# Performance work log

Hardware: AMD Instinct MI355X
Metric: run time of the kernel (lower is better)

The kernel has to match this reference:

```python
import jax, jax.numpy as jnp
import numpy as np

# ---- hyperparameters (from args defaults) ----
TEMPERATURE = 0.07
ALPHA = 0.5
OT_EPSILON = 0.1
OT_ITERS = 20
HOLO_WEIGHT = 1.0
RKD_DISTANCE_WEIGHT = 1.0
RKD_ANGLE_WEIGHT = 2.0
GLOBAL_RKD_WEIGHT = 10.0
MATRYOSHKA_DIMS = [128, 768]
MATRYOSHKA_WEIGHTS = [1.0, 2.0]

B, N, H_S, H_T, D_REP = 64, 256, 768, 1024, 768


def l2norm(x, axis=-1):
    # F.normalize(p=2): x / max(||x||, eps)
    n = jnp.sqrt(jnp.sum(x * x, axis=axis, keepdims=True))
    return x / jnp.maximum(n, 1e-12)


def pairwise_distance(x):
    # [n, d] -> [n, n] squared-euclidean-style distances
    sq = jnp.sum(x * x, axis=1, keepdims=True)
    return sq + sq.T - 2.0 * (x @ x.T)


def huber(diff):
    a = jnp.abs(diff)
    return jnp.where(a < 1.0, 0.5 * a * a, a - 0.5)


def rkd_distance_loss(s, t):
    n = s.shape[0]
    mask = jnp.triu(jnp.ones((n, n), dtype=bool), k=1)
    cnt = jnp.sum(mask.astype(s.dtype))
    ds, dt = pairwise_distance(s), pairwise_distance(t)
    mean_s = jax.lax.stop_gradient(jnp.sum(jnp.where(mask, ds, 0.0)) / cnt) + 1e-8
    mean_t = jax.lax.stop_gradient(jnp.sum(jnp.where(mask, dt, 0.0)) / cnt) + 1e-8
    loss = huber(ds / mean_s - dt / mean_t)
    return jnp.sum(jnp.where(mask, loss, 0.0)) / cnt


def angle_potentials(x):
    # diffs[i, j] = x[j] - x[i]
    diffs = x[None, :, :] - x[:, None, :]
    e = diffs / (jnp.linalg.norm(diffs, axis=-1, keepdims=True) + 1e-8)
    return jnp.einsum('ijd,kjd->ijk', e, e)


def rkd_angle_loss(s, t):
    psi_s, psi_t = angle_potentials(s), angle_potentials(t)
    n = psi_s.shape[0]
    idx = jnp.arange(n)
    i, j, k = idx[:, None, None], idx[None, :, None], idx[None, None, :]
    mask = (i != j) & (i != k) & (j != k)  # exclude degenerate triplets
    cnt = jnp.sum(mask.astype(s.dtype))
    loss = huber(psi_s - psi_t)
    return jnp.sum(jnp.where(mask, loss, 0.0)) / cnt


def saliency_measure(h, temp=1.0):
    # softmax over token axis of hidden-state norms -> [B, N, 1]
    norms = jnp.linalg.norm(h, axis=-1)
    return jax.nn.softmax(norms / temp, axis=-1)[..., None]


def structure_matrix(z):
    zn = l2norm(z, axis=-1)
    return 1.0 - jnp.einsum('bnd,bmd->bnm', zn, zn)


def sinkhorn_knopp_log_domain(C, mu, nu):
    # C: [B, Ns, Nt]; mu: [B, Ns, 1]; nu: [B, Nt, 1]
    log_K = -C / OT_EPSILON
    log_mu = jnp.log(mu + 1e-8)
    log_nu = jnp.log(nu + 1e-8)
    u = jnp.zeros_like(mu)
    v = jnp.zeros_like(nu)
    for _ in range(OT_ITERS):
        u = log_mu - jax.scipy.special.logsumexp(
            log_K + jnp.swapaxes(v, 1, 2), axis=2, keepdims=True)
        v = log_nu - jax.scipy.special.logsumexp(
            jnp.swapaxes(log_K, 1, 2) + jnp.swapaxes(u, 1, 2),
            axis=2, keepdims=True)
    return jnp.exp(u + log_K + jnp.swapaxes(v, 1, 2))


def fused_gromov_wasserstein(z_s, z_t, proj_w, proj_b):
    mu = saliency_measure(z_s)   # [B, N, 1]
    nu = saliency_measure(z_t)   # [B, N, 1]
    C_s = structure_matrix(z_s)  # [B, N, N]
    C_t = structure_matrix(z_t)
    z_s_norm = l2norm(z_s @ proj_w + proj_b, axis=-1)
    z_t_norm = l2norm(z_t, axis=-1)
    M = 1.0 - jnp.einsum('bnd,bmd->bnm', z_s_norm, z_t_norm)
    Gamma = sinkhorn_knopp_log_domain(M, mu, nu)
    feat_loss = jnp.mean(jnp.sum(M * Gamma, axis=(1, 2)))
    Gamma_norm = Gamma / (jnp.sum(Gamma, axis=2, keepdims=True) + 1e-8)
    C_t_mapped = jnp.einsum('bnm,bmk,blk->bnl', Gamma_norm, C_t, Gamma_norm)
    w = jnp.einsum('bni,bmi->bnm', mu, mu)  # mu @ mu^T
    struct_loss = jnp.mean(jnp.sum((C_s - C_t_mapped) ** 2 * w, axis=(1, 2)))
    return (1.0 - ALPHA) * feat_loss + ALPHA * struct_loss


def cross_entropy_inbatch(scores):
    # labels = arange(B)
    logZ = jax.scipy.special.logsumexp(scores, axis=1)
    return jnp.mean(logZ - jnp.diagonal(scores))


def setup_inputs() -> dict:
    key = jax.random.key(0)
    ks = jax.random.split(key, 10)
    return {
        's_q_reps': jax.random.normal(ks[0], (B, D_REP), jnp.float32),
        's_p_reps': jax.random.normal(ks[1], (B, D_REP), jnp.float32),
        't_q_reps': jax.random.normal(ks[2], (B, D_REP), jnp.float32),
        't_p_reps': jax.random.normal(ks[3], (B, D_REP), jnp.float32),
        's_q_states': jax.random.normal(ks[4], (B, N, H_S), jnp.float32),
        's_p_states': jax.random.normal(ks[5], (B, N, H_S), jnp.float32),
        't_q_states': jax.random.normal(ks[6], (B, N, H_T), jnp.float32),
        't_p_states': jax.random.normal(ks[7], (B, N, H_T), jnp.float32),
        'proj_w': jax.random.normal(ks[8], (H_S, H_T), jnp.float32) * (H_S ** -0.5),
        'proj_b': jnp.zeros((H_T,), jnp.float32),
    }


def reference(s_q_reps, s_p_reps, t_q_reps, t_p_reps,
              s_q_states, s_p_states, t_q_states, t_p_states,
              proj_w, proj_b):
    # teacher outputs are computed under torch.no_grad()
    t_q_reps = jax.lax.stop_gradient(t_q_reps)
    t_p_reps = jax.lax.stop_gradient(t_p_reps)
    t_q_states = jax.lax.stop_gradient(t_q_states)
    t_p_states = jax.lax.stop_gradient(t_p_states)

    contrastive_acc = 0.0
    holo_acc = 0.0
    rkd_acc = 0.0
    for dim, dim_weight in zip(MATRYOSHKA_DIMS, MATRYOSHKA_WEIGHTS):
        s_q_slice = l2norm(s_q_reps[:, :dim])
        s_p_slice = l2norm(s_p_reps[:, :dim])
        scores = (s_q_slice @ s_p_slice.T) / TEMPERATURE
        contrastive_acc += dim_weight * cross_entropy_inbatch(scores)
        if dim <= 128:
            s_batch = jnp.concatenate([s_q_slice, s_p_slice], axis=0)
            t_batch = jnp.concatenate(
                [l2norm(t_q_reps[:, :dim]), l2norm(t_p_reps[:, :dim])], axis=0)
            loss_dist = rkd_distance_loss(s_batch, t_batch)
            loss_angle = rkd_angle_loss(s_batch, t_batch)
            rkd_val = (RKD_DISTANCE_WEIGHT * loss_dist
                       + RKD_ANGLE_WEIGHT * loss_angle)
            rkd_acc += GLOBAL_RKD_WEIGHT * rkd_val * 2.0
        else:
            loss_q = fused_gromov_wasserstein(s_q_states, t_q_states, proj_w, proj_b)
            loss_p = fused_gromov_wasserstein(s_p_states, t_p_states, proj_w, proj_b)
            holo_acc += HOLO_WEIGHT * 0.5 * (loss_q + loss_p)
    return contrastive_acc + holo_acc + rkd_acc
```

## Files before the change

kernel.cpp:

```cpp
#include <hip/hip_runtime.h>
#include <math.h>

#define NB   64
#define NN   256
#define HSS  768
#define HTT  1024
#define ROWS (NB*NN)
#define C2LOG 14.426950408889634f

typedef unsigned short u16;
typedef __attribute__((ext_vector_type(8))) short bf16x8;
typedef __attribute__((ext_vector_type(4))) float f32x4;

#define LIDX(r,c) (((r)<<8) + (((((c)>>3) + (r)) & 31)<<3) + ((c)&7))
#define EIDX(r,c) (((r)<<7) + (((((c)>>3) + (r)) & 15)<<3) + ((c)&7))

__device__ __forceinline__ void gl16(const u16* g, u16* l){
  __builtin_amdgcn_global_load_lds(
      (const __attribute__((address_space(1))) unsigned int*)g,
      (__attribute__((address_space(3))) unsigned int*)l,
      16, 0, 0);
}

static const size_t OFF_ACC   = 0;
static const size_t OFF_SQ128 = 16;
static const size_t OFF_SP128 = OFF_SQ128 + 64*128;
static const size_t OFF_TQ128 = OFF_SP128 + 64*128;
static const size_t OFF_TP128 = OFF_TQ128 + 64*128;
static const size_t OFF_SQ768 = OFF_TP128 + 64*128;
static const size_t OFF_SP768 = OFF_SQ768 + 64*768;
static const size_t OFF_DS    = OFF_SP768 + 64*768;
static const size_t OFF_DT    = OFF_DS + 128*128;
static const size_t OFF_CS    = OFF_DT + 128*128;
static const size_t OFF_MBF   = OFF_CS  + (size_t)2*NB*NN*NN;
static const size_t OFF_ZS_BF = OFF_MBF + (size_t)NB*NN*NN;
static const size_t OFF_ZT_BF = OFF_ZS_BF + (size_t)ROWS*HSS/2;
static const size_t OFF_WT_BF = OFF_ZT_BF + (size_t)ROWS*HTT/2;
static const size_t OFF_ZSP_BF= OFF_WT_BF + (size_t)HTT*HSS/2;
static const size_t OFF_GN_BF = OFF_ZSP_BF+ (size_t)ROWS*HTT/2;
static const size_t OFF_CT_BF = OFF_GN_BF + (size_t)NB*NN*NN;
static const size_t OFF_T_BF  = OFF_ZS_BF;
static const size_t OFF_NS    = OFF_CT_BF + (size_t)NB*NN*NN;
static const size_t OFF_NT    = OFF_NS + ROWS;
static const size_t OFF_MU    = OFF_NT + ROWS;
static const size_t OFF_NU    = OFF_MU + 2*ROWS;
static const size_t OFF_NSPP  = OFF_NU + 2*ROWS;


__device__ __forceinline__ float wred_sum(float v){
  #pragma unroll
  for(int o=32;o>0;o>>=1) v += __shfl_xor(v,o,64);
  return v;
}
__device__ __forceinline__ float wred_max(float v){
  #pragma unroll
  for(int o=32;o>0;o>>=1) v = fmaxf(v, __shfl_xor(v,o,64));
  return v;
}
__device__ __forceinline__ u16 f2bf(float f){
  unsigned u = __float_as_uint(f);
  unsigned r = (u + 0x7fffu + ((u>>16)&1u)) >> 16;
  return (u16)r;
}
__device__ __forceinline__ float bf2f(u16 h){
  return __uint_as_float(((unsigned)h)<<16);
}

__global__ __launch_bounds__(256) void k_l2norm_all(
    const float* __restrict__ sq, const float* __restrict__ sp,
    const float* __restrict__ tq, const float* __restrict__ tp,
    float* __restrict__ ws){
  int bid = blockIdx.x;
  int r = bid & 63;
  const float* in; float* out; int kuse;
  if(bid < 64)       { in = sq; out = ws + OFF_SQ128; kuse = 128; }
  else if(bid < 128) { in = sp; out = ws + OFF_SP128; kuse = 128; }
  else if(bid < 192) { in = tq; out = ws + OFF_TQ128; kuse = 128; }
  else if(bid < 256) { in = tp; out = ws + OFF_TP128; kuse = 128; }
  else if(bid < 320) { in = sq; out = ws + OFF_SQ768; kuse = 768; }
  else               { in = sp; out = ws + OFF_SP768; kuse = 768; }
  const float* row = in + (size_t)r*768;
  float ss = 0.f;
  for(int d=threadIdx.x; d<kuse; d+=256){ float x=row[d]; ss += x*x; }
  ss = wred_sum(ss);
  __shared__ float sm[4];
  if((threadIdx.x&63)==0) sm[threadIdx.x>>6]=ss;
  __syncthreads();
  float tot = sm[0]+sm[1]+sm[2]+sm[3];
  float inv = 1.f / fmaxf(sqrtf(tot), 1e-12f);
  for(int d=threadIdx.x; d<kuse; d+=256) out[(size_t)r*kuse + d] = row[d]*inv;
}

__global__ __launch_bounds__(512) void k_contrastive2(const float* __restrict__ ws,
    float* __restrict__ acc){
  int bid = blockIdx.x;
  int i = bid & 63;
  int big = bid >> 6;
  const float* q = ws + (big ? OFF_SQ768 : OFF_SQ128);
  const float* p = ws + (big ? OFF_SP768 : OFF_SP128);
  int dim = big ? 768 : 128;
  float weight = big ? 2.f : 1.f;
  int j = threadIdx.x & 63;
  int part = threadIdx.x >> 6;
  const float* qi = q + (size_t)i*dim;
  const float* pj = p + (size_t)j*dim;
  int seg = dim >> 3;
  int d0 = part*seg;
  float dot = 0.f;
  for(int d=d0; d<d0+seg; d+=4){
    float4 a = *(const float4*)(qi+d);
    float4 b = *(const float4*)(pj+d);
    dot = fmaf(a.x,b.x,dot);
    dot = fmaf(a.y,b.y,dot);
    dot = fmaf(a.z,b.z,dot);
    dot = fmaf(a.w,b.w,dot);
  }
  __shared__ float sm[8][64];
  sm[part][j] = dot;
  __syncthreads();
  if(part==0){
    float s = 0.f;
    #pragma unroll
    for(int k=0;k<8;k++) s += sm[k][j];
    s = s / 0.07f;
    float mx = wred_max(s);
    float e = expf(s - mx);
    float Z = wred_sum(e);
    float logZ = mx + logf(Z);
    float diag = __shfl(s, i, 64);
    if(j==0) atomicAdd(acc+0, weight*(logZ - diag)*(1.f/64.f));
  }
}

__global__ __launch_bounds__(256) void k_pack_cvt(
    const float* __restrict__ zs, const float* __restrict__ zt,
    u16* __restrict__ zsb, u16* __restrict__ ztb,
    float* __restrict__ ns, float* __restrict__ nt,
    const float* __restrict__ sb128, const float* __restrict__ tb128,
    float* __restrict__ ds, float* __restrict__ dt, float* __restrict__ acc)
{
  __shared__ float sm[2][2];
  int bid = blockIdx.x;
  if(bid < 8192){
    const float* in; u16* out; float* nrm; int K; int cb;
    if(bid < 4096){ in=zs; out=zsb; nrm=ns; K=HSS; cb=bid; }
    else          { in=zt; out=ztb; nrm=nt; K=HTT; cb=bid-4096; }
    int w = threadIdx.x >> 6, l = threadIdx.x & 63;
    int r = cb*4 + w;
    const float* row = in + (size_t)r*K;
    u16* orow = out + (size_t)r*K;
    float ss = 0.f;
    int nv = K >> 8;
    for(int i=0;i<nv;i++){
      int d = l*4 + i*256;
      float4 x = *(const float4*)(row + d);
      ushort4 o; o.x=f2bf(x.x); o.y=f2bf(x.y); o.z=f2bf(x.z); o.w=f2bf(x.w);
      *(ushort4*)(orow + d) = o;
      ss += x.x*x.x + x.y*x.y + x.z*x.z + x.w*x.w;
    }
    ss = wred_sum(ss);
    if(l==0) nrm[r] = sqrtf(ss);
    return;
  }
  {
    int r = bid - 8192;
    int c = threadIdx.x;
    float ms = 0.f, mt = 0.f;
    if(c < 128){
      const float* sr = sb128 + r*128; const float* sc = sb128 + c*128;
      const float* tr = tb128 + r*128; const float* tc = tb128 + c*128;
      float dot_s=0,ssr=0,ssc=0,dot_t=0,tsr=0,tsc=0;
      for(int d=0; d<128; d++){
        float a=sr[d], bb=sc[d]; dot_s += a*bb; ssr += a*a; ssc += bb*bb;
        float at=tr[d], bt=tc[d]; dot_t += at*bt; tsr += at*at; tsc += bt*bt;
      }
      float dv = ssr + ssc - 2.f*dot_s;
      float tv = tsr + tsc - 2.f*dot_t;
      ds[r*128+c] = dv; dt[r*128+c] = tv;
      ms = (c>r)? dv : 0.f;
      mt = (c>r)? tv : 0.f;
      ms = wred_sum(ms); mt = wred_sum(mt);
      if((c&63)==0){ sm[0][c>>6]=ms; sm[1][c>>6]=mt; }
    }
    __syncthreads();
    if(threadIdx.x==0){
      atomicAdd(acc+1, sm[0][0]+sm[0][1]);
      atomicAdd(acc+2, sm[1][0]+sm[1][1]);
    }
  }
}

__global__ __launch_bounds__(256) void k_small0(
    const float* __restrict__ ds, const float* __restrict__ dt,
    const float* __restrict__ ns, const float* __restrict__ nt,
    float* __restrict__ omu, float* __restrict__ onu, float* __restrict__ acc)
{
  __shared__ float sm[4], sm2[4];
  int bid = blockIdx.x;
  if(bid < 128){
    int r = bid, c = threadIdx.x;
    float mean_s = acc[1]*(1.f/8128.f) + 1e-8f;
    float mean_t = acc[2]*(1.f/8128.f) + 1e-8f;
    float h = 0.f;
    if(c < 128){
      if(c > r){
        float diff = ds[r*128+c]/mean_s - dt[r*128+c]/mean_t;
        float a = fabsf(diff);
        h = (a<1.f)? 0.5f*a*a : a-0.5f;
      }
      h = wred_sum(h);
      if((c&63)==0) sm[c>>6]=h;
    }
    __syncthreads();
    if(threadIdx.x==0) atomicAdd(acc+3, sm[0]+sm[1]);
    return;
  }
  {
    int b0 = bid - 128, n = threadIdx.x;
    const float* nrm = (b0 < NB) ? ns : nt;
    float* out = (b0 < NB) ? omu : onu;
    int b = b0 & 63;
    float x = nrm[b*NN+n];
    float mx = wred_max(x);
    if((n&63)==0) sm[n>>6]=mx;
    __syncthreads();
    mx = fmaxf(fmaxf(sm[0],sm[1]),fmaxf(sm[2],sm[3]));
    float e = expf(x-mx);
    float s = wred_sum(e);
    if((n&63)==0) sm2[n>>6]=s;
    __syncthreads();
    s = sm2[0]+sm2[1]+sm2[2]+sm2[3];
    out[b*NN+n] = e/s;
  }
}

#define RKD_LDS 65536
__global__ __launch_bounds__(256, 1) void k_rkd_angle_mfma(
    const float* __restrict__ sb, const float* __restrict__ tb,
    float* __restrict__ accp)
{
  extern __shared__ u16 eSh[];
  u16* Es = eSh;
  u16* Et = eSh + 128*128;
  const int j    = blockIdx.x >> 1;
  const int half = blockIdx.x & 1;
  const int tid = threadIdx.x;
  {
    const int i = tid >> 1, h = tid & 1;
    #pragma unroll
    for(int which=0; which<2; which++){
      const float* xb = which ? tb : sb;
      u16* E = which ? Et : Es;
      const float* xj = xb + j*128 + h*64;
      const float* xi = xb + i*128 + h*64;
      float ss = 0.f;
      #pragma unroll
      for(int d4=0; d4<16; d4++){
        float4 a = *(const float4*)(xj + d4*4);
        float4 b = *(const float4*)(xi + d4*4);
        float d0=a.x-b.x, d1=a.y-b.y, d2=a.z-b.z, d3=a.w-b.w;
        ss += d0*d0+d1*d1+d2*d2+d3*d3;
      }
      ss += __shfl_xor(ss, 1, 64);
      float inv = (i==j) ? 0.f : 1.f/(sqrtf(ss)+1e-8f);
      #pragma unroll
      for(int d4=0; d4<16; d4++){
        float4 a = *(const float4*)(xj + d4*4);
        float4 b = *(const float4*)(xi + d4*4);
        int c = h*64 + d4*4;
        E[EIDX(i,c+0)] = f2bf((a.x-b.x)*inv);
        E[EIDX(i,c+1)] = f2bf((a.y-b.y)*inv);
        E[EIDX(i,c+2)] = f2bf((a.z-b.z)*inv);
        E[EIDX(i,c+3)] = f2bf((a.w-b.w)*inv);
      }
    }
  }
  __syncthreads();
  const int w = tid >> 6, lane = tid & 63;
  const int q = lane >> 4, loc = lane & 15;
  float hsum = 0.f;
  #pragma unroll
  for(int ni=0; ni<4; ni++){
    const int cb = half*64 + ni*16;
    #pragma unroll
    for(int mi=0; mi<2; mi++){
      const int rb = w*32 + mi*16;
      f32x4 as_ = {0.f,0.f,0.f,0.f}, at_ = {0.f,0.f,0.f,0.f};
      #pragma unroll
      for(int k0=0; k0<128; k0+=32){
        int ra = rb + loc, rbn = cb + loc;
        int ca = k0 + q*8;
        bf16x8 aS = *(const bf16x8*)(Es + EIDX(ra, ca));
        bf16x8 bS = *(const bf16x8*)(Es + EIDX(rbn, ca));
        bf16x8 aT = *(const bf16x8*)(Et + EIDX(ra, ca));
        bf16x8 bT = *(const bf16x8*)(Et + EIDX(rbn, ca));
        as_ = __builtin_amdgcn_mfma_f32_16x16x32_bf16(aS, bS, as_, 0,0,0);
        at_ = __builtin_amdgcn_mfma_f32_16x16x32_bf16(aT, bT, at_, 0,0,0);
      }
      #pragma unroll
      for(int jj=0; jj<4; jj++){
        int row = rb + q*4 + jj, col = cb + loc;
        if(row != col){
          float d = as_[jj] - at_[jj];
          float a = fabsf(d);
          hsum += (a < 1.f) ? 0.5f*a*a : a - 0.5f;
        }
      }
    }
  }
  hsum = wred_sum(hsum);
  __syncthreads();
  float* red = (float*)eSh;
  if(lane==0) red[w] = hsum;
  __syncthreads();
  if(tid==0) atomicAdd(accp+4, red[0]+red[1]+red[2]+red[3]);
}

__global__ void k_wt(const float* __restrict__ W, u16* __restrict__ Wt){
  __shared__ float t[32][33];
  int k0 = blockIdx.y*32, n0 = blockIdx.x*32;
  int tx = threadIdx.x, ty = threadIdx.y;
  for(int r=0;r<32;r+=8) t[ty+r][tx] = W[(size_t)(k0+ty+r)*HTT + n0+tx];
  __syncthreads();
  for(int r=0;r<32;r+=8) Wt[(size_t)(n0+ty+r)*HSS + k0+tx] = f2bf(t[tx][ty+r]);
}

__global__ __launch_bounds__(256) void k_saliency2(const float* __restrict__ ns,
    const float* __restrict__ nt, float* __restrict__ omu, float* __restrict__ onu){
  int b0 = blockIdx.x, n = threadIdx.x;
  const float* nrm = (b0 < NB) ? ns : nt;
  float* out = (b0 < NB) ? omu : onu;
  int b = b0 & 63;
  float x = nrm[b*NN+n];
  float mx = wred_max(x);
  __shared__ float sm[4], sm2[4];
  if((n&63)==0) sm[n>>6]=mx;
  __syncthreads();
  mx = fmaxf(fmaxf(sm[0],sm[1]),fmaxf(sm[2],sm[3]));
  float e = expf(x-mx);
  float s = wred_sum(e);
  if((n&63)==0) sm2[n>>6]=s;
  __syncthreads();
  s = sm2[0]+sm2[1]+sm2[2]+sm2[3];
  out[b*NN+n] = e/s;
}

__global__ __launch_bounds__(256) void k_proj(
    const u16* __restrict__ A, const u16* __restrict__ B,
    u16* __restrict__ outB, const float* __restrict__ bias,
    float* __restrict__ nspp)
{
  __shared__ u16 As[128*32];
  __shared__ u16 Bs[128*32];

  int gx = gridDim.x, gy = gridDim.y;
  int flat = blockIdx.x + gx*blockIdx.y;
  int nwg  = gx*gy;
  int cpx  = nwg >> 3;
  int lg   = (flat & 7)*cpx + (flat >> 3);
  int bx   = lg % gx;
  int by   = lg / gx;

  int tid = threadIdx.x;
  int lane = tid & 63, w = tid >> 6;
  int m0 = by*128, n0 = bx*128;
  int row_off = (w>>1)*64, col_off = (w&1)*64;
  int q = lane>>4, loc = lane&15;
  f32x4 acc[4][4] = {};

  const int srow = (lane >> 2);
  const int sslot = lane & 3;

  for(int k0=0;k0<HSS;k0+=32){
    #pragma unroll
    for(int h=0;h<2;h++){
      int row = h*64 + w*16 + srow;
      int ca  = (sslot ^ ((row>>1)&3))*8;
      u16* ldst = As + h*2048 + w*512 + lane*8;
      u16* ldstB= Bs + h*2048 + w*512 + lane*8;
      gl16(A + (size_t)(m0+row)*HSS + k0 + ca, ldst);
      gl16(B + (size_t)(n0+row)*HSS + k0 + ca, ldstB);
    }
    __syncthreads();
    bf16x8 af[4], bfr[4];
    #pragma unroll
    for(int mi=0;mi<4;mi++){
      int r = row_off + mi*16 + loc;
      int slot = q ^ ((r>>1)&3);
      af[mi] = *(const bf16x8*)(As + r*32 + slot*8);
    }
    #pragma unroll
    for(int ni=0;ni<4;ni++){
      int r = col_off + ni*16 + loc;
      int slot = q ^ ((r>>1)&3);
      bfr[ni] = *(const bf16x8*)(Bs + r*32 + slot*8);
    }
    #pragma unroll
    for(int mi=0;mi<4;mi++)
      #pragma unroll
      for(int ni=0;ni<4;ni++)
        acc[mi][ni] = __builtin_amdgcn_mfma_f32_16x16x32_bf16(af[mi], bfr[ni], acc[mi][ni], 0,0,0);
    __syncthreads();
  }

  int slice = bx*2 + (w&1);
  #pragma unroll
  for(int mi=0;mi<4;mi++){
    #pragma unroll
    for(int j=0;j<4;j++){
      int row = m0 + row_off + mi*16 + q*4 + j;
      float sq = 0.f;
      #pragma unroll
      for(int ni=0;ni<4;ni++){
        int col = n0 + col_off + ni*16 + loc;
        float v = acc[mi][ni][j] + bias[col];
        u16 h = f2bf(v);
        outB[(size_t)row*HTT + col] = h;
        float vq = bf2f(h);
        sq = fmaf(vq, vq, sq);
      }
      sq += __shfl_xor(sq, 1, 64);
      sq += __shfl_xor(sq, 2, 64);
      sq += __shfl_xor(sq, 4, 64);
      sq += __shfl_xor(sq, 8, 64);
      if(loc==0) nspp[(size_t)slice*ROWS + row] = sq;
    }
  }
}

enum { MODE_PROJ=0, MODE_COST=1, MODE_PLAIN=2, MODE_STRUCT=3 };

template<int MODE>
__global__ __launch_bounds__(256) void k_mfma64(
    const u16* __restrict__ A, int lda, long bA,
    const u16* __restrict__ B, int ldb, long bB,
    int K,
    float* __restrict__ outF, u16* __restrict__ outB, int ldo, long bO,
    const float* __restrict__ nx, const float* __restrict__ ny,
    const float* __restrict__ bias,
    const float* __restrict__ Cs, const float* __restrict__ mu,
    float* __restrict__ accp)
{
  __shared__ u16 As[64*32];
  __shared__ u16 Bs[64*32];
  __shared__ float red[4];

  int gx = gridDim.x, gy = gridDim.y;
  int flat = blockIdx.x + gx*(blockIdx.y + gy*blockIdx.z);
  int nwg  = gx*gy*gridDim.z;
  int cpx  = nwg >> 3;
  int lg   = (flat & 7)*cpx + (flat >> 3);
  int bx   = lg % gx;
  int rest = lg / gx;
  int by   = rest % gy;
  int b    = rest / gy;

  const u16* Ab = A + (size_t)b*bA;
  const u16* Bb = B + (size_t)b*bB;
  int tid = threadIdx.x;
  int lane = tid & 63, w = tid >> 6;
  int m0 = by*64, n0 = bx*64;
  int row_off = (w>>1)*32, col_off = (w&1)*32;
  int q = lane>>4, loc = lane&15;
  f32x4 acc[2][2] = {};

  const int srow = tid >> 2;
  const int sslot = tid & 3;

  for(int k0=0;k0<K;k0+=32){
    {
      int row = srow;
      int ca  = (sslot ^ ((row>>1)&3))*8;
      u16* la = As + w*512 + lane*8;
      u16* lb = Bs + w*512 + lane*8;
      gl16(Ab + (size_t)(m0+row)*lda + k0 + ca, la);
      gl16(Bb + (size_t)(n0+row)*ldb + k0 + ca, lb);
    }
    __syncthreads();
    bf16x8 af[2], bfr[2];
    #pragma unroll
    for(int mi=0;mi<2;mi++){
      int r = row_off + mi*16 + loc;
      int slot = q ^ ((r>>1)&3);
      af[mi] = *(const bf16x8*)(As + r*32 + slot*8);
    }
    #pragma unroll
    for(int ni=0;ni<2;ni++){
      int r = col_off + ni*16 + loc;
      int slot = q ^ ((r>>1)&3);
      bfr[ni] = *(const bf16x8*)(Bs + r*32 + slot*8);
    }
    #pragma unroll
    for(int mi=0;mi<2;mi++)
      #pragma unroll
      for(int ni=0;ni<2;ni++)
        acc[mi][ni] = __builtin_amdgcn_mfma_f32_16x16x32_bf16(af[mi], bfr[ni], acc[mi][ni], 0,0,0);
    __syncthreads();
  }

  float* outFb = outF ? outF + (size_t)b*bO : nullptr;
  u16*   outBb = outB ? outB + (size_t)b*bO : nullptr;
  const float* nxb = nx ? nx + (size_t)b*NN : nullptr;
  const float* nyb = ny ? ny + (size_t)b*NN : nullptr;
  const float* Cb  = (MODE==MODE_STRUCT) ? Cs + (size_t)b*bO : nullptr;
  const float* mb  = (MODE==MODE_STRUCT) ? mu + (size_t)b*NN : nullptr;
  float lsum = 0.f;
  #pragma unroll
  for(int mi=0;mi<2;mi++){
    #pragma unroll
    for(int j=0;j<4;j++){
      int row = m0 + row_off + mi*16 + q*4 + j;
      float ir = 0.f, mr = 0.f;
      if(MODE==MODE_COST)   ir = 1.f/fmaxf(nxb[row],1e-12f);
      if(MODE==MODE_STRUCT) mr = mb[row];
      #pragma unroll
      for(int ni=0;ni<2;ni++){
        int col = n0 + col_off + ni*16 + loc;
        float v = acc[mi][ni][j];
        if(MODE==MODE_COST){
          float ic = 1.f/fmaxf(nyb[col],1e-12f);
          v = 1.f - v*ir*ic;
          if(outFb) outFb[(size_t)row*ldo + col] = v;
          if(outBb) outBb[(size_t)row*ldo + col] = f2bf(v);
        } else if(MODE==MODE_PLAIN){
          outBb[(size_t)row*ldo + col] = f2bf(v);
        } else if(MODE==MODE_STRUCT){
          float d = Cb[(size_t)row*ldo + col] - v;
          lsum += d*d*mr*mb[col];
        }
      }
    }
  }
  if(MODE==MODE_STRUCT){
    lsum = wred_sum(lsum);
    if(lane==0) red[w] = lsum;
    __syncthreads();
    if(tid==0) atomicAdd(accp+6, red[0]+red[1]+red[2]+red[3]);
  }
}

__global__ __launch_bounds__(256) void k_mfma64_dual(
    const u16* __restrict__ A1, const u16* __restrict__ A2,
    const u16* __restrict__ B, int ld, long bStr,
    int K,
    u16* __restrict__ out1, u16* __restrict__ out2, long bO,
    const float* __restrict__ n1, const float* __restrict__ nspp,
    const float* __restrict__ ny)
{
  __shared__ u16 A1s[64*32];
  __shared__ u16 A2s[64*32];
  __shared__ u16 Bs[64*32];

  int gx = gridDim.x, gy = gridDim.y;
  int flat = blockIdx.x + gx*(blockIdx.y + gy*blockIdx.z);
  int nwg  = gx*gy*gridDim.z;
  int cpx  = nwg >> 3;
  int lg   = (flat & 7)*cpx + (flat >> 3);
  int bx   = lg % gx;
  int rest = lg / gx;
  int by   = rest % gy;
  int b    = rest / gy;

  const u16* A1b = A1 + (size_t)b*bStr;
  const u16* A2b = A2 + (size_t)b*bStr;
  const u16* Bb  = B  + (size_t)b*bStr;
  int tid = threadIdx.x;
  int lane = tid & 63, w = tid >> 6;
  int m0 = by*64, n0 = bx*64;
  int row_off = (w>>1)*32, col_off = (w&1)*32;
  int q = lane>>4, loc = lane&15;
  f32x4 acc1[2][2] = {};
  f32x4 acc2[2][2] = {};

  const int srow = tid >> 2;
  const int sslot = tid & 3;

  for(int k0=0;k0<K;k0+=32){
    {
      int row = srow;
      int ca  = (sslot ^ ((row>>1)&3))*8;
      u16* l1 = A1s + w*512 + lane*8;
      u16* l2 = A2s + w*512 + lane*8;
      u16* lb = Bs  + w*512 + lane*8;
      gl16(A1b + (size_t)(m0+row)*ld + k0 + ca, l1);
      gl16(A2b + (size_t)(m0+row)*ld + k0 + ca, l2);
      gl16(Bb  + (size_t)(n0+row)*ld + k0 + ca, lb);
    }
    __syncthreads();
    bf16x8 a1f[2], a2f[2], bfr[2];
    #pragma unroll
    for(int mi=0;mi<2;mi++){
      int r = row_off + mi*16 + loc;
      int slot = q ^ ((r>>1)&3);
      a1f[mi] = *(const bf16x8*)(A1s + r*32 + slot*8);
      a2f[mi] = *(const bf16x8*)(A2s + r*32 + slot*8);
    }
    #pragma unroll
    for(int ni=0;ni<2;ni++){
      int r = col_off + ni*16 + loc;
      int slot = q ^ ((r>>1)&3);
      bfr[ni] = *(const bf16x8*)(Bs + r*32 + slot*8);
    }
    #pragma unroll
    for(int mi=0;mi<2;mi++)
      #pragma unroll
      for(int ni=0;ni<2;ni++){
        acc1[mi][ni] = __builtin_amdgcn_mfma_f32_16x16x32_bf16(a1f[mi], bfr[ni], acc1[mi][ni], 0,0,0);
        acc2[mi][ni] = __builtin_amdgcn_mfma_f32_16x16x32_bf16(a2f[mi], bfr[ni], acc2[mi][ni], 0,0,0);
      }
    __syncthreads();
  }

  u16* o1 = out1 + (size_t)b*bO;
  u16* o2 = out2 + (size_t)b*bO;
  const float* n1b = n1 + (size_t)b*NN;
  const float* nyb = ny + (size_t)b*NN;
  #pragma unroll
  for(int mi=0;mi<2;mi++){
    #pragma unroll
    for(int j=0;j<4;j++){
      int row = m0 + row_off + mi*16 + q*4 + j;
      float ir1 = 1.f/fmaxf(n1b[row],1e-12f);
      size_t gr = (size_t)b*NN + row;
      float ssq = 0.f;
      #pragma unroll
      for(int s=0;s<16;s++) ssq += nspp[(size_t)s*ROWS + gr];
      float ir2 = 1.f/fmaxf(sqrtf(ssq),1e-12f);
      #pragma unroll
      for(int ni=0;ni<2;ni++){
        int col = n0 + col_off + ni*16 + loc;
        float ic = 1.f/fmaxf(nyb[col],1e-12f);
        float v1 = 1.f - acc1[mi][ni][j]*ir1*ic;
        float v2 = 1.f - acc2[mi][ni][j]*ir2*ic;
        o1[(size_t)row*NN + col] = f2bf(v1);
        o2[(size_t)row*NN + col] = f2bf(v2);
      }
    }
  }
}

#define SINK_DYN_LDS 131072
__global__ __launch_bounds__(1024, 1) void k_sink_cs(
    const u16* __restrict__ Mbf, const float* __restrict__ muL,
    const float* __restrict__ nuL, u16* __restrict__ Gn, float* __restrict__ accp,
    const u16* __restrict__ ZS, const float* __restrict__ ns,
    float* __restrict__ CsOut)
{
  extern __shared__ u16 dynLds[];
  __shared__ __align__(16) float part[4096];
  __shared__ __align__(16) float su[NN], sv[NN], smu[NN], snu[NN];
  __shared__ float red[16];

  const int bid = blockIdx.x;
  const int t = threadIdx.x;

  if(bid >= 128){
    const int sub = t >> 8;
    const int st  = t & 255;
    int job = (bid - 128)*4 + sub;
    int bx = job & 3, by = (job >> 2) & 3, b = job >> 4;
    const u16* Ab = ZS + (size_t)b*NN*HSS;
    u16* As = dynLds + (size_t)sub*4096;
    u16* Bs = As + 2048;
    int lane = st & 63, w = st >> 6;
    int m0 = by*64, n0 = bx*64;
    int row_off = (w>>1)*32, col_off = (w&1)*32;
    int q = lane>>4, loc = lane&15;
    f32x4 acc[2][2] = {};
    const int srow = st >> 2;
    const int sslot = st & 3;

    for(int k0=0;k0<HSS;k0+=32){
      {
        int row = srow;
        int ca  = (sslot ^ ((row>>1)&3))*8;
        gl16(Ab + (size_t)(m0+row)*HSS + k0 + ca, As + w*512 + lane*8);
        gl16(Ab + (size_t)(n0+row)*HSS + k0 + ca, Bs + w*512 + lane*8);
      }
      __syncthreads();
      bf16x8 af[2], bfr[2];
      #pragma unroll
      for(int mi=0;mi<2;mi++){
        int r = row_off + mi*16 + loc;
        int slot = q ^ ((r>>1)&3);
        af[mi] = *(const bf16x8*)(As + r*32 + slot*8);
      }
      #pragma unroll
      for(int ni=0;ni<2;ni++){
        int r = col_off + ni*16 + loc;
        int slot = q ^ ((r>>1)&3);
        bfr[ni] = *(const bf16x8*)(Bs + r*32 + slot*8);
      }
      #pragma unroll
      for(int mi=0;mi<2;mi++)
        #pragma unroll
        for(int ni=0;ni<2;ni++)
          acc[mi][ni] = __builtin_amdgcn_mfma_f32_16x16x32_bf16(af[mi], bfr[ni], acc[mi][ni], 0,0,0);
      __syncthreads();
    }

    float* outFb = CsOut + (size_t)b*NN*NN;
    const float* nb = ns + (size_t)b*NN;
    #pragma unroll
    for(int mi=0;mi<2;mi++){
      #pragma unroll
      for(int j=0;j<4;j++){
        int row = m0 + row_off + mi*16 + q*4 + j;
        float ir = 1.f/fmaxf(nb[row],1e-12f);
        #pragma unroll
        for(int ni=0;ni<2;ni++){
          int col = n0 + col_off + ni*16 + loc;
          float ic = 1.f/fmaxf(nb[col],1e-12f);
          float v = 1.f - acc[mi][ni][j]*ir*ic;
          outFb[(size_t)row*NN + col] = v;
        }
      }
    }
    return;
  }

  u16* Ks = dynLds;
  const int b = bid;
  const u16* Mb = Mbf + (size_t)b*NN*NN;

  #pragma unroll
  for(int i=0;i<16;i++){
    int e = (i*1024 + t)*4;
    int r = e>>8, c = e&255;
    ushort4 mv = *(const ushort4*)(Mb + e);
    ushort4 o;
    o.x = f2bf(exp2f(-C2LOG*bf2f(mv.x)));
    o.y = f2bf(exp2f(-C2LOG*bf2f(mv.y)));
    o.z = f2bf(exp2f(-C2LOG*bf2f(mv.z)));
    o.w = f2bf(exp2f(-C2LOG*bf2f(mv.w)));
    *(ushort4*)(Ks + LIDX(r,c)) = o;
  }
  if(t < NN){
    smu[t] = muL[(size_t)b*NN+t] + 1e-8f;
    snu[t] = nuL[(size_t)b*NN+t] + 1e-8f;
    sv[t] = 1.f;
  }
  __syncthreads();

  const int r_ = t & 255, p_ = t >> 8;
  const int w = t>>6, l = t&63;

  for(int it=0; it<20; it++){
    {
      float s0=0.f, s1=0.f, s2=0.f, s3=0.f;
      #pragma unroll
      for(int jj=0;jj<8;jj++){
        int c0 = p_*64 + jj*8;
        uint4 kv = *(const uint4*)(Ks + LIDX(r_, c0));
        float4 va = *(const float4*)(sv + c0);
        float4 vb = *(const float4*)(sv + c0 + 4);
        s0 = fmaf(__uint_as_float(kv.x<<16),           va.x, s0);
        s1 = fmaf(__uint_as_float(kv.x & 0xffff0000u), va.y, s1);
        s2 = fmaf(__uint_as_float(kv.y<<16),           va.z, s2);
        s3 = fmaf(__uint_as_float(kv.y & 0xffff0000u), va.w, s3);
        s0 = fmaf(__uint_as_float(kv.z<<16),           vb.x, s0);
        s1 = fmaf(__uint_as_float(kv.z & 0xffff0000u), vb.y, s1);
        s2 = fmaf(__uint_as_float(kv.w<<16),           vb.z, s2);
        s3 = fmaf(__uint_as_float(kv.w & 0xffff0000u), vb.w, s3);
      }
      part[t] = (s0+s1)+(s2+s3);
    }
    __syncthreads();
    if(t < NN){
      float S = part[t] + part[256+t] + part[512+t] + part[768+t];
      su[t] = smu[t] / S;
    }
    __syncthreads();
    {
      float cs0=0.f,cs1=0.f,cs2=0.f,cs3=0.f;
      #pragma unroll
      for(int rr=0;rr<16;rr++){
        int r = w*16 + rr;
        ushort4 kv = *(const ushort4*)(Ks + LIDX(r, l*4));
        float ur = su[r];
        cs0 = fmaf(bf2f(kv.x), ur, cs0);
        cs1 = fmaf(bf2f(kv.y), ur, cs1);
        cs2 = fmaf(bf2f(kv.z), ur, cs2);
        cs3 = fmaf(bf2f(kv.w), ur, cs3);
      }
      float4 o; o.x=cs0; o.y=cs1; o.z=cs2; o.w=cs3;
      *(float4*)(part + w*256 + l*4) = o;
    }
    __syncthreads();
    if(t < NN){
      float S = 0.f;
      #pragma unroll
      for(int ww=0;ww<16;ww++) S += part[ww*256 + t];
      sv[t] = snu[t] / S;
    }
    __syncthreads();
  }

  {
    float s0=0.f, s1=0.f, s2=0.f, s3=0.f;
    #pragma unroll
    for(int jj=0;jj<8;jj++){
      int c0 = p_*64 + jj*8;
      uint4 kv = *(const uint4*)(Ks + LIDX(r_, c0));
      float4 va = *(const float4*)(sv + c0);
      float4 vb = *(const float4*)(sv + c0 + 4);
      s0 = fmaf(__uint_as_float(kv.x<<16),           va.x, s0);
      s1 = fmaf(__uint_as_float(kv.x & 0xffff0000u), va.y, s1);
      s2 = fmaf(__uint_as_float(kv.y<<16),           va.z, s2);
      s3 = fmaf(__uint_as_float(kv.y & 0xffff0000u), va.w, s3);
      s0 = fmaf(__uint_as_float(kv.z<<16),           vb.x, s0);
      s1 = fmaf(__uint_as_float(kv.z & 0xffff0000u), vb.y, s1);
      s2 = fmaf(__uint_as_float(kv.w<<16),           vb.z, s2);
      s3 = fmaf(__uint_as_float(kv.w & 0xffff0000u), vb.w, s3);
    }
    part[t] = (s0+s1)+(s2+s3);
  }
  __syncthreads();
  if(t < NN){
    float S = part[t] + part[256+t] + part[512+t] + part[768+t];
    smu[t] = 1.f / (su[t]*S + 1e-8f);
  }
  __syncthreads();

  u16* Gb = Gn + (size_t)b*NN*NN;
  const float IC = -1.f/C2LOG;
  float v0 = sv[l*4+0], v1 = sv[l*4+1], v2 = sv[l*4+2], v3 = sv[l*4+3];
  float fl = 0.f;
  for(int rr=0;rr<16;rr++){
    int r = w*16 + rr;
    ushort4 kv = *(const ushort4*)(Ks + LIDX(r, l*4));
    float k0=bf2f(kv.x), k1=bf2f(kv.y), k2=bf2f(kv.z), k3=bf2f(kv.w);
    float ur = su[r], inv = smu[r];
    float g0=ur*k0*v0, g1=ur*k1*v1, g2=ur*k2*v2, g3=ur*k3*v3;
    fl += g0*(__log2f(k0)*IC) + g1*(__log2f(k1)*IC)
        + g2*(__log2f(k2)*IC) + g3*(__log2f(k3)*IC);
    ushort4 o;
    o.x=f2bf(g0*inv); o.y=f2bf(g1*inv); o.z=f2bf(g2*inv); o.w=f2bf(g3*inv);
    *(ushort4*)(Gb + (size_t)r*NN + l*4) = o;
  }
  fl = wred_sum(fl);
  if(l==0) red[w] = fl;
  __syncthreads();
  if(t==0){
    float s=0.f;
    #pragma unroll
    for(int i=0;i<16;i++) s+=red[i];
    atomicAdd(accp+5, s);
  }
}

__global__ void k_final(const float* __restrict__ acc, float* __restrict__ out){
  out[0] = acc[0]
         + 20.f*acc[3]*(1.f/8128.f)
         + 40.f*acc[4]*(1.f/2048256.f)
         + 0.25f*(acc[5]+acc[6])*(1.f/64.f);
}

extern "C" void kernel_launch(void* const* d_in, const int* in_sizes, int n_in,
                              void* d_out, int out_size, void* d_ws, size_t ws_size,
                              hipStream_t stream) {
  const float* s_q_reps   = (const float*)d_in[0];
  const float* s_p_reps   = (const float*)d_in[1];
  const float* t_q_reps   = (const float*)d_in[2];
  const float* t_p_reps   = (const float*)d_in[3];
  const float* s_q_states = (const float*)d_in[4];
  const float* s_p_states = (const float*)d_in[5];
  const float* t_q_states = (const float*)d_in[6];
  const float* t_p_states = (const float*)d_in[7];
  const float* proj_w     = (const float*)d_in[8];
  const float* proj_b     = (const float*)d_in[9];
  float* ws = (float*)d_ws;
  float* acc = ws + OFF_ACC;
  u16* M_BF   = (u16*)(ws + OFF_MBF);
  u16* ZS_BF  = (u16*)(ws + OFF_ZS_BF);
  u16* ZT_BF  = (u16*)(ws + OFF_ZT_BF);
  u16* WT_BF  = (u16*)(ws + OFF_WT_BF);
  u16* ZSP_BF = (u16*)(ws + OFF_ZSP_BF);
  u16* GN_BF  = (u16*)(ws + OFF_GN_BF);
  u16* CT_BF  = (u16*)(ws + OFF_CT_BF);
  u16* T_BF   = (u16*)(ws + OFF_T_BF);

  hipFuncSetAttribute(reinterpret_cast<const void*>(k_sink_cs),
                      hipFuncAttributeMaxDynamicSharedMemorySize, SINK_DYN_LDS);
  hipFuncSetAttribute(reinterpret_cast<const void*>(k_rkd_angle_mfma),
                      hipFuncAttributeMaxDynamicSharedMemorySize, RKD_LDS);

  hipMemsetAsync(acc, 0, 16*sizeof(float), stream);

  k_l2norm_all<<<384,256,0,stream>>>(s_q_reps, s_p_reps, t_q_reps, t_p_reps, ws);
  k_contrastive2<<<128,512,0,stream>>>(ws, acc);

  k_pack_cvt<<<8320,256,0,stream>>>(s_q_states, t_q_states, ZS_BF, ZT_BF,
      ws+OFF_NS, ws+OFF_NT, ws+OFF_SQ128, ws+OFF_TQ128, ws+OFF_DS, ws+OFF_DT, acc);
  k_small0<<<256,256,0,stream>>>(ws+OFF_DS, ws+OFF_DT, ws+OFF_NS, ws+OFF_NT,
      ws+OFF_MU, ws+OFF_NU, acc);
  k_rkd_angle_mfma<<<256,256,RKD_LDS,stream>>>(ws+OFF_SQ128, ws+OFF_TQ128, acc);
  k_wt<<<dim3(HTT/32, HSS/32),dim3(32,8),0,stream>>>(proj_w, WT_BF);

  for(int pass=0; pass<2; pass++){
    size_t po  = (size_t)pass*NB*NN*NN;
    size_t pr  = (size_t)pass*ROWS;
    if(pass==1){
      k_pack_cvt<<<8192,256,0,stream>>>(s_p_states, t_p_states, ZS_BF, ZT_BF,
          ws+OFF_NS, ws+OFF_NT, ws+OFF_SQ128, ws+OFF_TQ128, ws+OFF_DS, ws+OFF_DT, acc);
      k_saliency2<<<128,256,0,stream>>>(ws+OFF_NS, ws+OFF_NT, ws+OFF_MU+pr, ws+OFF_NU+pr);
    }
    k_proj<<<dim3(HTT/128, ROWS/128),256,0,stream>>>(
        ZS_BF, WT_BF, ZSP_BF, proj_b, ws+OFF_NSPP);
    if(pass==0){
      k_mfma64<MODE_COST><<<dim3(4,4,NB),256,0,stream>>>(
          ZS_BF, HSS, (long)NN*HSS, ZS_BF, HSS, (long)NN*HSS, HSS,
          ws+OFF_CS+po, nullptr, NN, (long)NN*NN,
          ws+OFF_NS, ws+OFF_NS, nullptr, nullptr, nullptr, nullptr);
    }
    k_mfma64_dual<<<dim3(4,4,NB),256,0,stream>>>(
        ZT_BF, ZSP_BF, ZT_BF, HTT, (long)NN*HTT, HTT,
        CT_BF+po, M_BF+po, (long)NN*NN,
        ws+OFF_NT, ws+OFF_NSPP, ws+OFF_NT);
  }

  k_sink_cs<<<384,1024,SINK_DYN_LDS,stream>>>(
      M_BF, ws+OFF_MU, ws+OFF_NU, GN_BF, acc,
      ZS_BF, ws+OFF_NS, ws+OFF_CS + (size_t)NB*NN*NN);

  k_mfma64<MODE_PLAIN><<<dim3(4,4,2*NB),256,0,stream>>>(
      GN_BF, NN, (long)NN*NN, CT_BF, NN, (long)NN*NN, NN,
      nullptr, T_BF, NN, (long)NN*NN,
      nullptr, nullptr, nullptr, nullptr, nullptr, nullptr);
  k_mfma64<MODE_STRUCT><<<dim3(4,4,2*NB),256,0,stream>>>(
      T_BF, NN, (long)NN*NN, GN_BF, NN, (long)NN*NN, NN,
      nullptr, nullptr, NN, (long)NN*NN,
      nullptr, nullptr, nullptr, ws+OFF_CS, ws+OFF_MU, acc);

  k_final<<<1,1,0,stream>>>(acc, (float*)d_out);
}
```

Before: 590.3 us.

## Fuse GW structure GEMM chain into one kernel and merge projection with cost GEMM

Replaces the two batched GEMM launches (Gn·Ct written to global as bf16, then T·Gn with a loss epilogue) with a single kernel per 64-row strip. That kernel keeps the intermediate 64x256 T tile in LDS and consumes it directly, avoiding the global round trip and one launch. It also merges the pass-0 projection GEMM and the source cosine-cost GEMM into one launch using block-index ranges, so both run concurrently. The tradeoffs are higher LDS use per block (about 50KB), fewer blocks for the structure stage, and recomputation of B-operand loads across the four strips.

```diff
diff --git a/kernel.cpp b/kernel.cpp
--- a/kernel.cpp
+++ b/kernel.cpp
@@ -39,7 +39,6 @@
 static const size_t OFF_ZSP_BF= OFF_WT_BF + (size_t)HTT*HSS/2;
 static const size_t OFF_GN_BF = OFF_ZSP_BF+ (size_t)ROWS*HTT/2;
 static const size_t OFF_CT_BF = OFF_GN_BF + (size_t)NB*NN*NN;
-static const size_t OFF_T_BF  = OFF_ZS_BF;
 static const size_t OFF_NS    = OFF_CT_BF + (size_t)NB*NN*NN;
 static const size_t OFF_NT    = OFF_NS + ROWS;
 static const size_t OFF_MU    = OFF_NT + ROWS;
@@ -428,114 +427,146 @@
   }
 }
 
-enum { MODE_PROJ=0, MODE_COST=1, MODE_PLAIN=2, MODE_STRUCT=3 };
-
-template<int MODE>
-__global__ __launch_bounds__(256) void k_mfma64(
-    const u16* __restrict__ A, int lda, long bA,
-    const u16* __restrict__ B, int ldb, long bB,
-    int K,
-    float* __restrict__ outF, u16* __restrict__ outB, int ldo, long bO,
-    const float* __restrict__ nx, const float* __restrict__ ny,
-    const float* __restrict__ bias,
-    const float* __restrict__ Cs, const float* __restrict__ mu,
-    float* __restrict__ accp)
+__global__ __launch_bounds__(256) void k_proj_cs(
+    const u16* __restrict__ ZS, const u16* __restrict__ WT,
+    u16* __restrict__ ZSP, const float* __restrict__ bias,
+    float* __restrict__ nspp,
+    const float* __restrict__ ns, float* __restrict__ CsOut)
 {
-  __shared__ u16 As[64*32];
-  __shared__ u16 Bs[64*32];
-  __shared__ float red[4];
-
-  int gx = gridDim.x, gy = gridDim.y;
-  int flat = blockIdx.x + gx*(blockIdx.y + gy*blockIdx.z);
-  int nwg  = gx*gy*gridDim.z;
-  int cpx  = nwg >> 3;
-  int lg   = (flat & 7)*cpx + (flat >> 3);
-  int bx   = lg % gx;
-  int rest = lg / gx;
-  int by   = rest % gy;
-  int b    = rest / gy;
-
-  const u16* Ab = A + (size_t)b*bA;
-  const u16* Bb = B + (size_t)b*bB;
+  __shared__ u16 sh[8192];
+  int bid = blockIdx.x;
   int tid = threadIdx.x;
   int lane = tid & 63, w = tid >> 6;
-  int m0 = by*64, n0 = bx*64;
-  int row_off = (w>>1)*32, col_off = (w&1)*32;
   int q = lane>>4, loc = lane&15;
-  f32x4 acc[2][2] = {};
-
-  const int srow = tid >> 2;
-  const int sslot = tid & 3;
-
-  for(int k0=0;k0<K;k0+=32){
-    {
-      int row = srow;
-      int ca  = (sslot ^ ((row>>1)&3))*8;
-      u16* la = As + w*512 + lane*8;
-      u16* lb = Bs + w*512 + lane*8;
-      gl16(Ab + (size_t)(m0+row)*lda + k0 + ca, la);
-      gl16(Bb + (size_t)(n0+row)*ldb + k0 + ca, lb);
-    }
-    __syncthreads();
-    bf16x8 af[2], bfr[2];
+
+  if(bid < 1024){
+    u16* As = sh;
+    u16* Bs = sh + 4096;
+    int f = bid;
+    int lg = (f & 7)*128 + (f >> 3);
+    int bx = lg % 8;
+    int by = lg / 8;
+    int m0 = by*128, n0 = bx*128;
+    int row_off = (w>>1)*64, col_off = (w&1)*64;
+    f32x4 acc[4][4] = {};
+    const int srow = (lane >> 2);
+    const int sslot = lane & 3;
+
+    for(int k0=0;k0<HSS;k0+=32){
+      #pragma unroll
+      for(int h=0;h<2;h++){
+        int row = h*64 + w*16 + srow;
+        int ca  = (sslot ^ ((row>>1)&3))*8;
+        gl16(ZS + (size_t)(m0+row)*HSS + k0 + ca, As + h*2048 + w*512 + lane*8);
+        gl16(WT + (size_t)(n0+row)*HSS + k0 + ca, Bs + h*2048 + w*512 + lane*8);
+      }
+      __syncthreads();
+      bf16x8 af[4], bfr[4];
+      #pragma unroll
+      for(int mi=0;mi<4;mi++){
+        int r = row_off + mi*16 + loc;
+        int slot = q ^ ((r>>1)&3);
+        af[mi] = *(const bf16x8*)(As + r*32 + slot*8);
+      }
+      #pragma unroll
+      for(int ni=0;ni<4;ni++){
+        int r = col_off + ni*16 + loc;
+        int slot = q ^ ((r>>1)&3);
+        bfr[ni] = *(const bf16x8*)(Bs + r*32 + slot*8);
+      }
+      #pragma unroll
+      for(int mi=0;mi<4;mi++)
+        #pragma unroll
+        for(int ni=0;ni<4;ni++)
+          acc[mi][ni] = __builtin_amdgcn_mfma_f32_16x16x32_bf16(af[mi], bfr[ni], acc[mi][ni], 0,0,0);
+      __syncthreads();
+    }
+
+    int slice = bx*2 + (w&1);
+    #pragma unroll
+    for(int mi=0;mi<4;mi++){
+      #pragma unroll
+      for(int j=0;j<4;j++){
+        int row = m0 + row_off + mi*16 + q*4 + j;
+        float sq = 0.f;
+        #pragma unroll
+        for(int ni=0;ni<4;ni++){
+          int col = n0 + col_off + ni*16 + loc;
+          float v = acc[mi][ni][j] + bias[col];
+          u16 h = f2bf(v);
+          ZSP[(size_t)row*HTT + col] = h;
+          float vq = bf2f(h);
+          sq = fmaf(vq, vq, sq);
+        }
+        sq += __shfl_xor(sq, 1, 64);
+        sq += __shfl_xor(sq, 2, 64);
+        sq += __shfl_xor(sq, 4, 64);
+        sq += __shfl_xor(sq, 8, 64);
+        if(loc==0) nspp[(size_t)slice*ROWS + row] = sq;
+      }
+    }
+    return;
+  }
+
+  {
+    u16* As = sh;
+    u16* Bs = sh + 2048;
+    int f = bid - 1024;
+    int lg = (f & 7)*128 + (f >> 3);
+    int bx = lg & 3, by = (lg >> 2) & 3, b = lg >> 4;
+    const u16* Ab = ZS + (size_t)b*NN*HSS;
+    int m0 = by*64, n0 = bx*64;
+    int row_off = (w>>1)*32, col_off = (w&1)*32;
+    f32x4 acc[2][2] = {};
+    const int srow = tid >> 2;
+    const int sslot = tid & 3;
+
+    for(int k0=0;k0<HSS;k0+=32){
+      {
+        int row = srow;
+        int ca  = (sslot ^ ((row>>1)&3))*8;
+        gl16(Ab + (size_t)(m0+row)*HSS + k0 + ca, As + w*512 + lane*8);
+        gl16(Ab + (size_t)(n0+row)*HSS + k0 + ca, Bs + w*512 + lane*8);
+      }
+      __syncthreads();
+      bf16x8 af[2], bfr[2];
+      #pragma unroll
+      for(int mi=0;mi<2;mi++){
+        int r = row_off + mi*16 + loc;
+        int slot = q ^ ((r>>1)&3);
+        af[mi] = *(const bf16x8*)(As + r*32 + slot*8);
+      }
+      #pragma unroll
+      for(int ni=0;ni<2;ni++){
+        int r = col_off + ni*16 + loc;
+        int slot = q ^ ((r>>1)&3);
+        bfr[ni] = *(const bf16x8*)(Bs + r*32 + slot*8);
+      }
+      #pragma unroll
+      for(int mi=0;mi<2;mi++)
+        #pragma unroll
+        for(int ni=0;ni<2;ni++)
+          acc[mi][ni] = __builtin_amdgcn_mfma_f32_16x16x32_bf16(af[mi], bfr[ni], acc[mi][ni], 0,0,0);
+      __syncthreads();
+    }
+
+    float* outFb = CsOut + (size_t)b*NN*NN;
+    const float* nb = ns + (size_t)b*NN;
     #pragma unroll
     for(int mi=0;mi<2;mi++){
-      int r = row_off + mi*16 + loc;
-      int slot = q ^ ((r>>1)&3);
-      af[mi] = *(const bf16x8*)(As + r*32 + slot*8);
-    }
-    #pragma unroll
-    for(int ni=0;ni<2;ni++){
-      int r = col_off + ni*16 + loc;
-      int slot = q ^ ((r>>1)&3);
-      bfr[ni] = *(const bf16x8*)(Bs + r*32 + slot*8);
-    }
-    #pragma unroll
-    for(int mi=0;mi<2;mi++)
-      #pragma unroll
-      for(int ni=0;ni<2;ni++)
-        acc[mi][ni] = __builtin_amdgcn_mfma_f32_16x16x32_bf16(af[mi], bfr[ni], acc[mi][ni], 0,0,0);
-    __syncthreads();
-  }
-
-  float* outFb = outF ? outF + (size_t)b*bO : nullptr;
-  u16*   outBb = outB ? outB + (size_t)b*bO : nullptr;
-  const float* nxb = nx ? nx + (size_t)b*NN : nullptr;
-  const float* nyb = ny ? ny + (size_t)b*NN : nullptr;
-  const float* Cb  = (MODE==MODE_STRUCT) ? Cs + (size_t)b*bO : nullptr;
-  const float* mb  = (MODE==MODE_STRUCT) ? mu + (size_t)b*NN : nullptr;
-  float lsum = 0.f;
-  #pragma unroll
-  for(int mi=0;mi<2;mi++){
-    #pragma unroll
-    for(int j=0;j<4;j++){
-      int row = m0 + row_off + mi*16 + q*4 + j;
-      float ir = 0.f, mr = 0.f;
-      if(MODE==MODE_COST)   ir = 1.f/fmaxf(nxb[row],1e-12f);
-      if(MODE==MODE_STRUCT) mr = mb[row];
-      #pragma unroll
-      for(int ni=0;ni<2;ni++){
-        int col = n0 + col_off + ni*16 + loc;
-        float v = acc[mi][ni][j];
-        if(MODE==MODE_COST){
-          float ic = 1.f/fmaxf(nyb[col],1e-12f);
-          v = 1.f - v*ir*ic;
-          if(outFb) outFb[(size_t)row*ldo + col] = v;
-          if(outBb) outBb[(size_t)row*ldo + col] = f2bf(v);
-        } else if(MODE==MODE_PLAIN){
-          outBb[(size_t)row*ldo + col] = f2bf(v);
-        } else if(MODE==MODE_STRUCT){
-          float d = Cb[(size_t)row*ldo + col] - v;
-          lsum += d*d*mr*mb[col];
+      #pragma unroll
+      for(int j=0;j<4;j++){
+        int row = m0 + row_off + mi*16 + q*4 + j;
+        float ir = 1.f/fmaxf(nb[row],1e-12f);
+        #pragma unroll
+        for(int ni=0;ni<2;ni++){
+          int col = n0 + col_off + ni*16 + loc;
+          float ic = 1.f/fmaxf(nb[col],1e-12f);
+          float v = 1.f - acc[mi][ni][j]*ir*ic;
+          outFb[(size_t)row*NN + col] = v;
         }
       }
     }
-  }
-  if(MODE==MODE_STRUCT){
-    lsum = wred_sum(lsum);
-    if(lane==0) red[w] = lsum;
-    __syncthreads();
-    if(tid==0) atomicAdd(accp+6, red[0]+red[1]+red[2]+red[3]);
   }
 }
 
@@ -579,12 +610,9 @@
     {
       int row = srow;
       int ca  = (sslot ^ ((row>>1)&3))*8;
-      u16* l1 = A1s + w*512 + lane*8;
-      u16* l2 = A2s + w*512 + lane*8;
-      u16* lb = Bs  + w*512 + lane*8;
-      gl16(A1b + (size_t)(m0+row)*ld + k0 + ca, l1);
-      gl16(A2b + (size_t)(m0+row)*ld + k0 + ca, l2);
-      gl16(Bb  + (size_t)(n0+row)*ld + k0 + ca, lb);
+      gl16(A1b + (size_t)(m0+row)*ld + k0 + ca, A1s + w*512 + lane*8);
+      gl16(A2b + (size_t)(m0+row)*ld + k0 + ca, A2s + w*512 + lane*8);
+      gl16(Bb  + (size_t)(n0+row)*ld + k0 + ca, Bs  + w*512 + lane*8);
     }
     __syncthreads();
     bf16x8 a1f[2], a2f[2], bfr[2];
@@ -637,6 +665,135 @@
       }
     }
   }
+}
+
+__global__ __launch_bounds__(256) void k_gw_struct(
+    const u16* __restrict__ Gn, const u16* __restrict__ Ct,
+    const float* __restrict__ Cs, const float* __restrict__ mu,
+    float* __restrict__ accp)
+{
+  __shared__ u16 As[64*32];
+  __shared__ u16 Bs[256*32];
+  __shared__ u16 Tl[64*256];
+  __shared__ float red[4];
+
+  int flat = blockIdx.x;
+  int lg = (flat & 7)*64 + (flat >> 3);
+  int strip = lg & 3;
+  int b = lg >> 2;
+
+  const u16* Gnb = Gn + (size_t)b*NN*NN;
+  const u16* Ctb = Ct + (size_t)b*NN*NN;
+  int tid = threadIdx.x;
+  int lane = tid & 63, w = tid >> 6;
+  int m0 = strip*64;
+  int q = lane>>4, loc = lane&15;
+  f32x4 acc[4][4] = {};
+  const int srow = tid >> 2;
+  const int sslot = tid & 3;
+
+  for(int k0=0;k0<NN;k0+=32){
+    {
+      int rowA = srow;
+      int caA = (sslot ^ ((rowA>>1)&3))*8;
+      gl16(Gnb + (size_t)(m0+rowA)*NN + k0 + caA, As + tid*8);
+      #pragma unroll
+      for(int h=0;h<4;h++){
+        int rowB = h*64 + srow;
+        int caB = (sslot ^ ((rowB>>1)&3))*8;
+        gl16(Ctb + (size_t)rowB*NN + k0 + caB, Bs + h*2048 + tid*8);
+      }
+    }
+    __syncthreads();
+    bf16x8 af[4], bfr[4];
+    #pragma unroll
+    for(int mi=0;mi<4;mi++){
+      int r = mi*16 + loc;
+      int slot = q ^ ((r>>1)&3);
+      af[mi] = *(const bf16x8*)(As + r*32 + slot*8);
+    }
+    #pragma unroll
+    for(int ni=0;ni<4;ni++){
+      int r = w*64 + ni*16 + loc;
+      int slot = q ^ ((r>>1)&3);
+      bfr[ni] = *(const bf16x8*)(Bs + r*32 + slot*8);
+    }
+    #pragma unroll
+    for(int mi=0;mi<4;mi++)
+      #pragma unroll
+      for(int ni=0;ni<4;ni++)
+        acc[mi][ni] = __builtin_amdgcn_mfma_f32_16x16x32_bf16(af[mi], bfr[ni], acc[mi][ni], 0,0,0);
+    __syncthreads();
+  }
+
+  #pragma unroll
+  for(int mi=0;mi<4;mi++){
+    #pragma unroll
+    for(int j=0;j<4;j++){
+      int row = mi*16 + q*4 + j;
+      #pragma unroll
+      for(int ni=0;ni<4;ni++){
+        int col = w*64 + ni*16 + loc;
+        Tl[LIDX(row,col)] = f2bf(acc[mi][ni][j]);
+      }
+    }
+    #pragma unroll
+    for(int ni=0;ni<4;ni++)
+      acc[mi][ni] = (f32x4){0.f,0.f,0.f,0.f};
+  }
+  __syncthreads();
+
+  for(int k0=0;k0<NN;k0+=32){
+    {
+      #pragma unroll
+      for(int h=0;h<4;h++){
+        int rowB = h*64 + srow;
+        int caB = (sslot ^ ((rowB>>1)&3))*8;
+        gl16(Gnb + (size_t)rowB*NN + k0 + caB, Bs + h*2048 + tid*8);
+      }
+    }
+    __syncthreads();
+    bf16x8 af[4], bfr[4];
+    #pragma unroll
+    for(int mi=0;mi<4;mi++){
+      int r = mi*16 + loc;
+      af[mi] = *(const bf16x8*)(Tl + LIDX(r, k0 + q*8));
+    }
+    #pragma unroll
+    for(int ni=0;ni<4;ni++){
+      int r = w*64 + ni*16 + loc;
+      int slot = q ^ ((r>>1)&3);
+      bfr[ni] = *(const bf16x8*)(Bs + r*32 + slot*8);
+    }
+    #pragma unroll
+    for(int mi=0;mi<4;mi++)
+      #pragma unroll
+      for(int ni=0;ni<4;ni++)
+        acc[mi][ni] = __builtin_amdgcn_mfma_f32_16x16x32_bf16(af[mi], bfr[ni], acc[mi][ni], 0,0,0);
+    __syncthreads();
+  }
+
+  const float* Csb = Cs + (size_t)b*NN*NN;
+  const float* mb  = mu + (size_t)b*NN;
+  float lsum = 0.f;
+  #pragma unroll
+  for(int mi=0;mi<4;mi++){
+    #pragma unroll
+    for(int j=0;j<4;j++){
+      int row = m0 + mi*16 + q*4 + j;
+      float mr = mb[row];
+      #pragma unroll
+      for(int ni=0;ni<4;ni++){
+        int col = w*64 + ni*16 + loc;
+        float d = Csb[(size_t)row*NN + col] - acc[mi][ni][j];
+        lsum += d*d*mr*mb[col];
+      }
+    }
+  }
+  lsum = wred_sum(lsum);
+  if(lane==0) red[w] = lsum;
+  __syncthreads();
+  if(tid==0) atomicAdd(accp+6, red[0]+red[1]+red[2]+red[3]);
 }
 
 #define SINK_DYN_LDS 131072
@@ -878,7 +1035,6 @@
   u16* ZSP_BF = (u16*)(ws + OFF_ZSP_BF);
   u16* GN_BF  = (u16*)(ws + OFF_GN_BF);
   u16* CT_BF  = (u16*)(ws + OFF_CT_BF);
-  u16* T_BF   = (u16*)(ws + OFF_T_BF);
 
   hipFuncSetAttribute(reinterpret_cast<const void*>(k_sink_cs),
                       hipFuncAttributeMaxDynamicSharedMemorySize, SINK_DYN_LDS);
@@ -897,22 +1053,22 @@
   k_rkd_angle_mfma<<<256,256,RKD_LDS,stream>>>(ws+OFF_SQ128, ws+OFF_TQ128, acc);
   k_wt<<<dim3(HTT/32, HSS/32),dim3(32,8),0,stream>>>(proj_w, WT_BF);
 
-  for(int pass=0; pass<2; pass++){
-    size_t po  = (size_t)pass*NB*NN*NN;
-    size_t pr  = (size_t)pass*ROWS;
-    if(pass==1){
-      k_pack_cvt<<<8192,256,0,stream>>>(s_p_states, t_p_states, ZS_BF, ZT_BF,
-          ws+OFF_NS, ws+OFF_NT, ws+OFF_SQ128, ws+OFF_TQ128, ws+OFF_DS, ws+OFF_DT, acc);
-      k_saliency2<<<128,256,0,stream>>>(ws+OFF_NS, ws+OFF_NT, ws+OFF_MU+pr, ws+OFF_NU+pr);
-    }
+  k_proj_cs<<<2048,256,0,stream>>>(
+      ZS_BF, WT_BF, ZSP_BF, proj_b, ws+OFF_NSPP,
+      ws+OFF_NS, ws+OFF_CS);
+  k_mfma64_dual<<<dim3(4,4,NB),256,0,stream>>>(
+      ZT_BF, ZSP_BF, ZT_BF, HTT, (long)NN*HTT, HTT,
+      CT_BF, M_BF, (long)NN*NN,
+      ws+OFF_NT, ws+OFF_NSPP, ws+OFF_NT);
+
+  {
+    size_t po  = (size_t)1*NB*NN*NN;
+    size_t pr  = (size_t)1*ROWS;
+    k_pack_cvt<<<8192,256,0,stream>>>(s_p_states, t_p_states, ZS_BF, ZT_BF,
+        ws+OFF_NS, ws+OFF_NT, ws+OFF_SQ128, ws+OFF_TQ128, ws+OFF_DS, ws+OFF_DT, acc);
+    k_saliency2<<<128,256,0,stream>>>(ws+OFF_NS, ws+OFF_NT, ws+OFF_MU+pr, ws+OFF_NU+pr);
     k_proj<<<dim3(HTT/128, ROWS/128),256,0,stream>>>(
         ZS_BF, WT_BF, ZSP_BF, proj_b, ws+OFF_NSPP);
-    if(pass==0){
-      k_mfma64<MODE_COST><<<dim3(4,4,NB),256,0,stream>>>(
-          ZS_BF, HSS, (long)NN*HSS, ZS_BF, HSS, (long)NN*HSS, HSS,
-          ws+OFF_CS+po, nullptr, NN, (long)NN*NN,
-          ws+OFF_NS, ws+OFF_NS, nullptr, nullptr, nullptr, nullptr);
-    }
     k_mfma64_dual<<<dim3(4,4,NB),256,0,stream>>>(
         ZT_BF, ZSP_BF, ZT_BF, HTT, (long)NN*HTT, HTT,
         CT_BF+po, M_BF+po, (long)NN*NN,
@@ -923,14 +1079,8 @@
       M_BF, ws+OFF_MU, ws+OFF_NU, GN_BF, acc,
       ZS_BF, ws+OFF_NS, ws+OFF_CS + (size_t)NB*NN*NN);
 
-  k_mfma64<MODE_PLAIN><<<dim3(4,4,2*NB),256,0,stream>>>(
-      GN_BF, NN, (long)NN*NN, CT_BF, NN, (long)NN*NN, NN,
-      nullptr, T_BF, NN, (long)NN*NN,
-      nullptr, nullptr, nullptr, nullptr, nullptr, nullptr);
-  k_mfma64<MODE_STRUCT><<<dim3(4,4,2*NB),256,0,stream>>>(
-      T_BF, NN, (long)NN*NN, GN_BF, NN, (long)NN*NN, NN,
-      nullptr, nullptr, NN, (long)NN*NN,
-      nullptr, nullptr, nullptr, ws+OFF_CS, ws+OFF_MU, acc);
+  k_gw_struct<<<512,256,0,stream>>>(
+      GN_BF, CT_BF, ws+OFF_CS, ws+OFF_MU, acc);
 
   k_final<<<1,1,0,stream>>>(acc, (float*)d_out);
 }
```

Result: faster. 547.2 us (-7.3%).
